# Performance work log

Hardware: AMD Instinct MI355X
Metric: run time of the kernel (lower is better)

Reference implementation:

```python
import jax, jax.numpy as jnp
import numpy as np

N_ROWS = 65536  # number of rows of the sparse input matrix


def setup_inputs() -> dict:
    key = jax.random.key(0)
    k1, k2, k3, k4, k5 = jax.random.split(key, 5)
    nnz, d_in, d_out = 524288, 512, 512
    rows = jax.random.randint(k1, (nnz,), 0, N_ROWS, dtype=jnp.int64)
    cols = jax.random.randint(k2, (nnz,), 0, d_in, dtype=jnp.int64)
    values = jax.random.normal(k3, (nnz,), dtype=jnp.float32)
    weight = jax.random.normal(k4, (d_out, d_in), dtype=jnp.float32) * (1.0 / np.sqrt(d_in))
    bound = 1.0 / np.sqrt(d_in)
    bias = jax.random.uniform(k5, (d_out,), minval=-bound, maxval=bound, dtype=jnp.float32)
    return {"rows": rows, "cols": cols, "values": values, "weight": weight, "bias": bias}


def reference(rows, cols, values, weight, bias):
    # y = sparse_input @ weight.T + bias
    # Each nonzero (r, c, v) contributes v * weight[:, c] to output row r.
    # weight: [d_out, d_in]; gather columns -> [nnz, d_out], segment-sum by row.
    contrib = values[:, None] * weight.T[cols]          # [nnz, d_out]
    y = jax.ops.segment_sum(contrib, rows, num_segments=N_ROWS)  # [N, d_out]
    return y + bias
```

## Files before the change

### kernel.cpp

```cpp
#include <hip/hip_runtime.h>
#include <hip/hip_bf16.h>

#define D 512
#define NROWS 65536
#define NBINS 256
#define RPB 128
#define P1B 1024
#define SEGCAP 16
#define MAXBLK1 512
#define HBINCAP 1408
#define OVFCAP 4096

typedef float f32x4 __attribute__((ext_vector_type(4)));

__global__ __launch_bounds__(256) void k_phase1(const float* __restrict__ w,
                                                __hip_bfloat16* __restrict__ wt,
                                                const int* __restrict__ rows,
                                                const int* __restrict__ cols,
                                                const float* __restrict__ vals, int nnz, int nblk1,
                                                uint2* __restrict__ gBin, int* __restrict__ gBinCnt,
                                                int* __restrict__ ovf_cnt, uint4* __restrict__ ovf) {
    int b = blockIdx.x, t = threadIdx.x;
    if (b < 256) {
        __shared__ float tile[32][33];
        int bx = b & 15, by = b >> 4;
        int tx = t & 31, ty = t >> 5;
        for (int i = ty; i < 32; i += 8)
            tile[i][tx] = w[(by * 32 + i) * D + bx * 32 + tx];
        __syncthreads();
        for (int i = ty; i < 32; i += 8)
            wt[(bx * 32 + i) * D + by * 32 + tx] = __float2bfloat16(tile[tx][i]);
        return;
    }
    __shared__ int  binCnt[NBINS];
    __shared__ uint2 binBuf[NBINS][SEGCAP];
    b -= 256;
    binCnt[t] = 0;
    __syncthreads();
    int base = b * P1B;
    int end = base + P1B; if (end > nnz) end = nnz;
    for (int i = base + t; i < end; i += 256) {
        int r = rows[i], c = cols[i];
        unsigned vb = __float_as_uint(vals[i]);
        int bin = r >> 8;
        int pos = atomicAdd(&binCnt[bin], 1);
        if (pos < SEGCAP) {
            binBuf[bin][pos] = make_uint2(((unsigned)r << 9) | (unsigned)c, vb);
        } else {
            int o = atomicAdd(ovf_cnt, 1);
            if (o < OVFCAP) ovf[o] = make_uint4((unsigned)r, (unsigned)c, vb, 0u);
        }
    }
    __syncthreads();
    for (int idx = t; idx < NBINS * SEGCAP; idx += 256) {
        int bin = idx >> 4, slot = idx & (SEGCAP - 1);
        int cnt = binCnt[bin]; if (cnt > SEGCAP) cnt = SEGCAP;
        if (slot < cnt)
            gBin[((size_t)b * NBINS + bin) * SEGCAP + slot] = binBuf[bin][slot];
        if (slot == 0) gBinCnt[b * NBINS + bin] = cnt;
    }
}

#define ACC8(wb, vv)                                   \
    do {                                               \
        f32x4 w0, w1;                                  \
        w0.x = __uint_as_float((wb).x << 16);          \
        w0.y = __uint_as_float((wb).x & 0xffff0000u);  \
        w0.z = __uint_as_float((wb).y << 16);          \
        w0.w = __uint_as_float((wb).y & 0xffff0000u);  \
        w1.x = __uint_as_float((wb).z << 16);          \
        w1.y = __uint_as_float((wb).z & 0xffff0000u);  \
        w1.z = __uint_as_float((wb).w << 16);          \
        w1.w = __uint_as_float((wb).w & 0xffff0000u);  \
        a0 += (vv) * w0;                               \
        a1 += (vv) * w1;                               \
    } while (0)

__global__ __launch_bounds__(512) void k_binspmm(const uint2* __restrict__ gBin,
                                                 const int* __restrict__ gBinCnt, int nblk1,
                                                 const uint4* __restrict__ wt4,
                                                 const f32x4* __restrict__ bias4,
                                                 f32x4* __restrict__ out,
                                                 int* __restrict__ ovf_cnt,
                                                 uint4* __restrict__ ovf) {
    __shared__ int segCnt[MAXBLK1];
    __shared__ int rowCnt[RPB], rowOff[RPB], cursor[RPB];
    __shared__ int wsum2[2];
    __shared__ int nPairs;
    __shared__ uint2 pairBuf[HBINCAP];
    __shared__ uint2 csrBuf[HBINCAP];
    int bin = blockIdx.x >> 1, half = blockIdx.x & 1;
    int t = threadIdx.x;
    int wv = t >> 6, lane = t & 63;
    segCnt[t] = (t < nblk1) ? gBinCnt[t * NBINS + bin] : 0;
    if (t < RPB) rowCnt[t] = 0;
    if (t == 0) nPairs = 0;
    __syncthreads();
    for (int idx = t; idx < nblk1 * SEGCAP; idx += 512) {
        int blk = idx >> 4, slot = idx & (SEGCAP - 1);
        if (slot < segCnt[blk]) {
            uint2 p = gBin[((size_t)blk * NBINS + bin) * SEGCAP + slot];
            int localr = (int)((p.x >> 9) & 255u);
            if ((localr >> 7) == half) {
                int dst = atomicAdd(&nPairs, 1);
                if (dst < HBINCAP) {
                    pairBuf[dst] = p;
                    atomicAdd(&rowCnt[localr & (RPB - 1)], 1);
                } else {
                    int o = atomicAdd(ovf_cnt, 1);
                    if (o < OVFCAP)
                        ovf[o] = make_uint4(p.x >> 9, p.x & 511u, p.y, 0u);
                }
            }
        }
    }
    __syncthreads();
    int total = nPairs; if (total > HBINCAP) total = HBINCAP;
    int rc = (t < RPB) ? rowCnt[t] : 0;
    int rx = rc;
    for (int d = 1; d < 64; d <<= 1) {
        int y = __shfl_up(rx, d, 64);
        if (lane >= d) rx += y;
    }
    if (t < RPB && lane == 63) wsum2[wv] = rx;
    __syncthreads();
    if (t < RPB) {
        int ro = rx - rc + ((wv == 1) ? wsum2[0] : 0);
        rowOff[t] = ro;
        cursor[t] = ro;
    }
    __syncthreads();
    for (int k = t; k < total; k += 512) {
        uint2 p = pairBuf[k];
        int r = (int)(p.x >> 9) & (RPB - 1);
        int pos = atomicAdd(&cursor[r], 1);
        csrBuf[pos] = make_uint2(p.x & 511u, p.y);
    }
    __syncthreads();
    f32x4 bb0 = bias4[lane * 2];
    f32x4 bb1 = bias4[lane * 2 + 1];
    int novf = *ovf_cnt;
    if (novf > OVFCAP) novf = OVFCAP;
    for (int rloc = wv; rloc < RPB; rloc += 8) {
        int cnt = rowCnt[rloc], o = rowOff[rloc];
        f32x4 a0 = bb0, a1 = bb1;
        for (int s = 0; s < cnt; s += 4) {
            int i1 = (s + 1 < cnt) ? s + 1 : s;
            int i2 = (s + 2 < cnt) ? s + 2 : s;
            int i3 = (s + 3 < cnt) ? s + 3 : s;
            uint2 p0 = csrBuf[o + s];
            uint2 p1 = csrBuf[o + i1];
            uint2 p2 = csrBuf[o + i2];
            uint2 p3 = csrBuf[o + i3];
            float v0 = __uint_as_float(p0.y);
            float v1 = (s + 1 < cnt) ? __uint_as_float(p1.y) : 0.f;
            float v2 = (s + 2 < cnt) ? __uint_as_float(p2.y) : 0.f;
            float v3 = (s + 3 < cnt) ? __uint_as_float(p3.y) : 0.f;
            uint4 wb0 = wt4[(size_t)p0.x * 64 + lane];
            uint4 wb1 = wt4[(size_t)p1.x * 64 + lane];
            uint4 wb2 = wt4[(size_t)p2.x * 64 + lane];
            uint4 wb3 = wt4[(size_t)p3.x * 64 + lane];
            ACC8(wb0, v0);
            ACC8(wb1, v1);
            ACC8(wb2, v2);
            ACC8(wb3, v3);
        }
        int row = (bin << 8) + (half << 7) + rloc;
        if (novf > 0) {
            for (int e = 0; e < novf; ++e) {
                uint4 p = ovf[e];
                if ((int)p.x == row) {
                    float v = __uint_as_float(p.z);
                    uint4 wb = wt4[(size_t)p.y * 64 + lane];
                    ACC8(wb, v);
                }
            }
        }
        f32x4* op = out + (size_t)row * (D / 4);
        op[lane * 2]     = a0;
        op[lane * 2 + 1] = a1;
    }
}

__global__ void k_init_bias(const float* __restrict__ bias, float* __restrict__ out, int total) {
    int i = blockIdx.x * blockDim.x + threadIdx.x;
    if (i < total) out[i] = bias[i & (D - 1)];
}

__global__ void k_atomic_spmm(const int* __restrict__ rows, const int* __restrict__ cols,
                              const float* __restrict__ vals, int nnz,
                              const float* __restrict__ w, float* __restrict__ out) {
    int wid = (int)((blockIdx.x * blockDim.x + threadIdx.x) >> 6);
    if (wid >= nnz) return;
    int lane = threadIdx.x & 63;
    int r = rows[wid];
    int c = cols[wid];
    float v = vals[wid];
    float* op = out + (size_t)r * D + lane * 8;
#pragma unroll
    for (int k = 0; k < 8; ++k) {
        float wv = w[(size_t)(lane * 8 + k) * D + c];
        atomicAdd(&op[k], v * wv);
    }
}

extern "C" void kernel_launch(void* const* d_in, const int* in_sizes, int n_in,
                              void* d_out, int out_size, void* d_ws, size_t ws_size,
                              hipStream_t stream) {
    const int*   rows   = (const int*)d_in[0];
    const int*   cols   = (const int*)d_in[1];
    const float* vals   = (const float*)d_in[2];
    const float* weight = (const float*)d_in[3];
    const float* bias   = (const float*)d_in[4];
    float*       out    = (float*)d_out;
    const int nnz = in_sizes[0];
    const int nblk1 = (nnz + P1B - 1) / P1B;

    char* ws = (char*)d_ws;
    size_t off = 0;
    auto alloc = [&](size_t bytes) -> void* {
        off = (off + 255) & ~(size_t)255;
        void* p = ws + off;
        off += bytes;
        return p;
    };
    __hip_bfloat16* wT = (__hip_bfloat16*)alloc((size_t)D * D * sizeof(__hip_bfloat16));
    int*   ovf_cnt = (int*)  alloc(256);
    uint4* ovf     = (uint4*)alloc((size_t)OVFCAP * sizeof(uint4));
    uint2* gBin    = (uint2*)alloc((size_t)MAXBLK1 * NBINS * SEGCAP * sizeof(uint2));
    int*   gBinCnt = (int*)  alloc((size_t)MAXBLK1 * NBINS * sizeof(int));
    const size_t need_full = off;

    if (need_full <= ws_size && nblk1 <= MAXBLK1) {
        hipMemsetAsync(ovf_cnt, 0, sizeof(int), stream);
        k_phase1<<<256 + nblk1, 256, 0, stream>>>(weight, wT, rows, cols, vals, nnz, nblk1,
                                                  gBin, gBinCnt, ovf_cnt, ovf);
        k_binspmm<<<NBINS * 2, 512, 0, stream>>>(gBin, gBinCnt, nblk1, (const uint4*)wT,
                                                 (const f32x4*)bias, (f32x4*)out, ovf_cnt, ovf);
    } else {
        k_init_bias<<<(out_size + 255) / 256, 256, 0, stream>>>(bias, out, out_size);
        k_atomic_spmm<<<((size_t)nnz * 64 + 255) / 256, 256, 0, stream>>>(rows, cols, vals, nnz, weight, out);
    }
}
```

Measured before the change: 64.27 us.

## Process whole bin per 1024-thread block with wave-aggregated pair compaction

Each bin is now handled by a single 1024-thread block covering all 256 rows, instead of two 512-thread blocks that each read the whole bin's segments and kept only their half. This removes the duplicated gBin reads and filtering. The per-pair atomicAdd on the shared counter becomes one atomic per wave, using ballot and popcount to give each lane its slot. The cost is twice the LDS per block and only 256 blocks, which may reduce occupancy and load balance across CUs.

```diff
diff --git a/kernel.cpp b/kernel.cpp
--- a/kernel.cpp
+++ b/kernel.cpp
@@ -4,11 +4,11 @@
 #define D 512
 #define NROWS 65536
 #define NBINS 256
-#define RPB 128
+#define RPB 256
 #define P1B 1024
 #define SEGCAP 16
 #define MAXBLK1 512
-#define HBINCAP 1408
+#define BINCAP 2816
 #define OVFCAP 4096
 
 typedef float f32x4 __attribute__((ext_vector_type(4)));
@@ -76,36 +76,43 @@
         a1 += (vv) * w1;                               \
     } while (0)
 
-__global__ __launch_bounds__(512) void k_binspmm(const uint2* __restrict__ gBin,
-                                                 const int* __restrict__ gBinCnt, int nblk1,
-                                                 const uint4* __restrict__ wt4,
-                                                 const f32x4* __restrict__ bias4,
-                                                 f32x4* __restrict__ out,
-                                                 int* __restrict__ ovf_cnt,
-                                                 uint4* __restrict__ ovf) {
+__global__ __launch_bounds__(1024) void k_binspmm(const uint2* __restrict__ gBin,
+                                                  const int* __restrict__ gBinCnt, int nblk1,
+                                                  const uint4* __restrict__ wt4,
+                                                  const f32x4* __restrict__ bias4,
+                                                  f32x4* __restrict__ out,
+                                                  int* __restrict__ ovf_cnt,
+                                                  uint4* __restrict__ ovf) {
     __shared__ int segCnt[MAXBLK1];
     __shared__ int rowCnt[RPB], rowOff[RPB], cursor[RPB];
-    __shared__ int wsum2[2];
+    __shared__ int wsum2[4];
     __shared__ int nPairs;
-    __shared__ uint2 pairBuf[HBINCAP];
-    __shared__ uint2 csrBuf[HBINCAP];
-    int bin = blockIdx.x >> 1, half = blockIdx.x & 1;
-    int t = threadIdx.x;
+    __shared__ uint2 pairBuf[BINCAP];
+    __shared__ uint2 csrBuf[BINCAP];
+    int bin = blockIdx.x, t = threadIdx.x;
     int wv = t >> 6, lane = t & 63;
-    segCnt[t] = (t < nblk1) ? gBinCnt[t * NBINS + bin] : 0;
+    if (t < MAXBLK1) segCnt[t] = (t < nblk1) ? gBinCnt[t * NBINS + bin] : 0;
     if (t < RPB) rowCnt[t] = 0;
     if (t == 0) nPairs = 0;
     __syncthreads();
-    for (int idx = t; idx < nblk1 * SEGCAP; idx += 512) {
+    for (int idx = t; idx < nblk1 * SEGCAP; idx += 1024) {
         int blk = idx >> 4, slot = idx & (SEGCAP - 1);
-        if (slot < segCnt[blk]) {
-            uint2 p = gBin[((size_t)blk * NBINS + bin) * SEGCAP + slot];
-            int localr = (int)((p.x >> 9) & 255u);
-            if ((localr >> 7) == half) {
-                int dst = atomicAdd(&nPairs, 1);
-                if (dst < HBINCAP) {
+        bool valid = slot < segCnt[blk];
+        uint2 p = make_uint2(0u, 0u);
+        if (valid) p = gBin[((size_t)blk * NBINS + bin) * SEGCAP + slot];
+        unsigned long long mask = __ballot(valid);
+        if (mask) {
+            int nActive = __popcll(mask);
+            int rank = __popcll(mask & ((1ULL << lane) - 1ULL));
+            int leader = (int)(__ffsll((long long)mask) - 1);
+            int basep = 0;
+            if (valid && rank == 0) basep = atomicAdd(&nPairs, nActive);
+            basep = __shfl(basep, leader);
+            if (valid) {
+                int dst = basep + rank;
+                if (dst < BINCAP) {
                     pairBuf[dst] = p;
-                    atomicAdd(&rowCnt[localr & (RPB - 1)], 1);
+                    atomicAdd(&rowCnt[(p.x >> 9) & (RPB - 1)], 1);
                 } else {
                     int o = atomicAdd(ovf_cnt, 1);
                     if (o < OVFCAP)
@@ -115,7 +122,7 @@
         }
     }
     __syncthreads();
-    int total = nPairs; if (total > HBINCAP) total = HBINCAP;
+    int total = nPairs; if (total > BINCAP) total = BINCAP;
     int rc = (t < RPB) ? rowCnt[t] : 0;
     int rx = rc;
     for (int d = 1; d < 64; d <<= 1) {
@@ -125,12 +132,16 @@
     if (t < RPB && lane == 63) wsum2[wv] = rx;
     __syncthreads();
     if (t < RPB) {
-        int ro = rx - rc + ((wv == 1) ? wsum2[0] : 0);
+        int pre = 0;
+#pragma unroll
+        for (int k = 0; k < 4; ++k)
+            if (k < wv) pre += wsum2[k];
+        int ro = rx - rc + pre;
         rowOff[t] = ro;
         cursor[t] = ro;
     }
     __syncthreads();
-    for (int k = t; k < total; k += 512) {
+    for (int k = t; k < total; k += 1024) {
         uint2 p = pairBuf[k];
         int r = (int)(p.x >> 9) & (RPB - 1);
         int pos = atomicAdd(&cursor[r], 1);
@@ -141,7 +152,7 @@
     f32x4 bb1 = bias4[lane * 2 + 1];
     int novf = *ovf_cnt;
     if (novf > OVFCAP) novf = OVFCAP;
-    for (int rloc = wv; rloc < RPB; rloc += 8) {
+    for (int rloc = wv; rloc < RPB; rloc += 16) {
         int cnt = rowCnt[rloc], o = rowOff[rloc];
         f32x4 a0 = bb0, a1 = bb1;
         for (int s = 0; s < cnt; s += 4) {
@@ -165,7 +176,7 @@
             ACC8(wb2, v2);
             ACC8(wb3, v3);
         }
-        int row = (bin << 8) + (half << 7) + rloc;
+        int row = (bin << 8) + rloc;
         if (novf > 0) {
             for (int e = 0; e < novf; ++e) {
                 uint4 p = ovf[e];
@@ -235,8 +246,8 @@
         hipMemsetAsync(ovf_cnt, 0, sizeof(int), stream);
         k_phase1<<<256 + nblk1, 256, 0, stream>>>(weight, wT, rows, cols, vals, nnz, nblk1,
                                                   gBin, gBinCnt, ovf_cnt, ovf);
-        k_binspmm<<<NBINS * 2, 512, 0, stream>>>(gBin, gBinCnt, nblk1, (const uint4*)wT,
-                                                 (const f32x4*)bias, (f32x4*)out, ovf_cnt, ovf);
+        k_binspmm<<<NBINS, 1024, 0, stream>>>(gBin, gBinCnt, nblk1, (const uint4*)wT,
+                                              (const f32x4*)bias, (f32x4*)out, ovf_cnt, ovf);
     } else {
         k_init_bias<<<(out_size + 255) / 256, 256, 0, stream>>>(bias, out, out_size);
         k_atomic_spmm<<<((size_t)nnz * 64 + 255) / 256, 256, 0, stream>>>(rows, cols, vals, nnz, weight, out);
```

After: 60.74 us. 1.06x faster.
